# Optimization experiments

Hardware: AMD Instinct MI355X
Metric: run time of the kernel (lower is better)

Reference implementation:

```python
import jax, jax.numpy as jnp
import numpy as np

EPS = 1e-10


def setup_inputs() -> dict:
    key = jax.random.key(0)
    k1, k2, k3 = jax.random.split(key, 3)
    B, K, M, X, Y = 32, 4, 3, 256, 256
    predictions = jax.random.uniform(k1, (B, K, X, Y), dtype=jnp.float32)
    inputs = jax.random.normal(k2, (B, M, X, Y), dtype=jnp.float32)
    heart = jax.random.randint(k3, (B, 1, X, Y), 0, 2, dtype=jnp.int32)
    return {"predictions": predictions, "inputs": inputs, "heart": heart}


def reference(predictions, inputs, heart):
    # predictions: [B,K,X,Y] soft class maps; inputs: [B,M,X,Y]; heart: [B,1,X,Y] 0/1 ROI
    mask = (heart[:, 0] == 1).astype(predictions.dtype)            # [B,X,Y]
    n = jnp.sum(mask, axis=(-2, -1))                                # [B] masked pixel count
    pred = predictions * mask[:, None]                              # [B,K,X,Y] zero outside ROI
    # alpha[b,k] = mean of pred over masked pixels
    alpha = jnp.sum(pred, axis=(-2, -1)) / n[:, None]               # [B,K]
    s = jnp.sum(pred, axis=(-2, -1)) + EPS                          # [B,K]
    # weighted means mu[b,k,m] = sum(pred*inp)/ (sum(pred)+eps)
    mu = jnp.einsum('bkxy,bmxy->bkm', pred, inputs) / s[:, :, None]  # [B,K,M]
    diff = inputs[:, None] - mu[:, :, :, None, None]                 # [B,K,M,X,Y]
    var = jnp.einsum('bkmxy,bkxy->bkm', diff * diff, pred) / s[:, :, None] + EPS  # [B,K,M]
    # Gaussian pdf per (k,m), product over channels m (done in log-space, same math)
    v = var[:, :, :, None, None]
    log_pdf = -0.5 * jnp.log(2.0 * jnp.pi * v) - (diff * diff) / (2.0 * v)  # [B,K,M,X,Y]
    g = jnp.exp(jnp.sum(log_pdf, axis=2))                            # [B,K,X,Y] = prod_m pdf
    mix = jnp.sum(alpha[:, :, None, None] * g, axis=1)               # [B,X,Y]
    ll = jnp.log(mix + EPS)                                          # [B,X,Y]
    # mean of -log-likelihood over masked pixels per batch, then mean over batch
    per_b = -jnp.sum(mask * ll, axis=(-2, -1)) / n                   # [B]
    return jnp.mean(per_b)
```

## Files before the change

kernel.cpp:

```cpp
#include <hip/hip_runtime.h>

#define EPSF 1e-10f

constexpr int B = 32, K = 4, M = 3;
constexpr int NPIX = 256 * 256;
constexpr int BLOCKS_PER_B = 8;
constexpr int THREADS = 256;
constexpr int WAVES = THREADS / 64;
constexpr int CHUNKS = NPIX / (BLOCKS_PER_B * THREADS * 4);
constexpr int NVALS = 1 + K + 2 * K * M;

constexpr int OFF_N     = 0;
constexpr int OFF_W     = OFF_N + B;
constexpr int OFF_P     = OFF_W + B * K;
constexpr int OFF_Q     = OFF_P + B * K * M;
constexpr int OFF_ALPHA = OFF_Q + B * K * M;
constexpr int OFF_MU    = OFF_ALPHA + B * K;
constexpr int OFF_IV    = OFF_MU + B * K * M;
constexpr int OFF_CST   = OFF_IV + B * K * M;
constexpr int OFF_LL    = OFF_CST + B * K;
constexpr int WS_FLOATS = OFF_LL + B;

__device__ __forceinline__ float wave_reduce(float v) {
    #pragma unroll
    for (int off = 32; off > 0; off >>= 1) v += __shfl_down(v, off, 64);
    return v;
}

__global__ __launch_bounds__(THREADS) void pass1_kernel(
    const float* __restrict__ pred, const float* __restrict__ xin,
    const int* __restrict__ heart, float* __restrict__ ws) {
    const int b  = blockIdx.x / BLOCKS_PER_B;
    const int cb = blockIdx.x % BLOCKS_PER_B;

    float nacc = 0.0f;
    float Wk[K] = {};
    float Pa[K][M] = {};
    float Qa[K][M] = {};

    for (int it = 0; it < CHUNKS; ++it) {
        const int p0 = (((cb * CHUNKS + it) * THREADS) + threadIdx.x) * 4;

        const int4 h4 = *(const int4*)(heart + b * NPIX + p0);
        float mk[4];
        mk[0] = (h4.x == 1) ? 1.0f : 0.0f;
        mk[1] = (h4.y == 1) ? 1.0f : 0.0f;
        mk[2] = (h4.z == 1) ? 1.0f : 0.0f;
        mk[3] = (h4.w == 1) ? 1.0f : 0.0f;
        nacc += (mk[0] + mk[1]) + (mk[2] + mk[3]);

        float xv[M][4];
        #pragma unroll
        for (int m = 0; m < M; ++m) {
            float4 t = *(const float4*)(xin + (b * M + m) * NPIX + p0);
            xv[m][0] = t.x; xv[m][1] = t.y; xv[m][2] = t.z; xv[m][3] = t.w;
        }

        #pragma unroll
        for (int k = 0; k < K; ++k) {
            float4 pr = *(const float4*)(pred + (b * K + k) * NPIX + p0);
            float pm[4];
            pm[0] = pr.x * mk[0]; pm[1] = pr.y * mk[1];
            pm[2] = pr.z * mk[2]; pm[3] = pr.w * mk[3];
            Wk[k] += (pm[0] + pm[1]) + (pm[2] + pm[3]);
            #pragma unroll
            for (int m = 0; m < M; ++m) {
                #pragma unroll
                for (int j = 0; j < 4; ++j) {
                    float px = pm[j] * xv[m][j];
                    Pa[k][m] += px;
                    Qa[k][m] += px * xv[m][j];
                }
            }
        }
    }

    float vals[NVALS];
    vals[0] = nacc;
    #pragma unroll
    for (int k = 0; k < K; ++k) vals[1 + k] = Wk[k];
    #pragma unroll
    for (int k = 0; k < K; ++k)
        #pragma unroll
        for (int m = 0; m < M; ++m) {
            vals[1 + K + k * M + m]         = Pa[k][m];
            vals[1 + K + K * M + k * M + m] = Qa[k][m];
        }

    __shared__ float red[WAVES * NVALS];
    #pragma unroll
    for (int i = 0; i < NVALS; ++i) vals[i] = wave_reduce(vals[i]);
    const int wave = threadIdx.x >> 6;
    if ((threadIdx.x & 63) == 0) {
        #pragma unroll
        for (int i = 0; i < NVALS; ++i) red[wave * NVALS + i] = vals[i];
    }
    __syncthreads();
    const int i = threadIdx.x;
    if (i < NVALS) {
        float s = red[i];
        #pragma unroll
        for (int w = 1; w < WAVES; ++w) s += red[w * NVALS + i];
        int dst;
        if (i == 0)            dst = OFF_N + b;
        else if (i < 1 + K)    dst = OFF_W + b * K + (i - 1);
        else if (i < 1 + K + K * M) dst = OFF_P + b * K * M + (i - 1 - K);
        else                   dst = OFF_Q + b * K * M + (i - 1 - K - K * M);
        atomicAdd(&ws[dst], s);
    }
}

__global__ __launch_bounds__(128) void params_kernel(float* __restrict__ ws) {
    const int t = threadIdx.x;
    if (t >= B * K) return;
    const int b = t / K;
    const float n = ws[OFF_N + b];
    const float W = ws[OFF_W + t];
    const float s = W + EPSF;
    ws[OFF_ALPHA + t] = W / n;
    float cst = 0.0f;
    #pragma unroll
    for (int m = 0; m < M; ++m) {
        const float Pv = ws[OFF_P + t * M + m];
        const float Qv = ws[OFF_Q + t * M + m];
        const float mu = Pv / s;
        const float var = (Qv - 2.0f * mu * Pv + mu * mu * W) / s + EPSF;
        ws[OFF_MU + t * M + m] = mu;
        ws[OFF_IV + t * M + m] = 0.5f / var;
        cst -= 0.5f * logf(6.2831853071795864f * var);
    }
    ws[OFF_CST + t] = cst;
}

__global__ __launch_bounds__(THREADS) void pass2_kernel(
    const float* __restrict__ xin, const int* __restrict__ heart,
    float* __restrict__ ws) {
    const int b  = blockIdx.x / BLOCKS_PER_B;
    const int cb = blockIdx.x % BLOCKS_PER_B;

    float alpha[K], cst[K], mu[K][M], iv[K][M];
    #pragma unroll
    for (int k = 0; k < K; ++k) {
        alpha[k] = ws[OFF_ALPHA + b * K + k];
        cst[k]   = ws[OFF_CST + b * K + k];
        #pragma unroll
        for (int m = 0; m < M; ++m) {
            mu[k][m] = ws[OFF_MU + (b * K + k) * M + m];
            iv[k][m] = ws[OFF_IV + (b * K + k) * M + m];
        }
    }

    float acc = 0.0f;
    for (int it = 0; it < CHUNKS; ++it) {
        const int p0 = (((cb * CHUNKS + it) * THREADS) + threadIdx.x) * 4;

        const int4 h4 = *(const int4*)(heart + b * NPIX + p0);
        int hv[4] = {h4.x, h4.y, h4.z, h4.w};

        float xv[M][4];
        #pragma unroll
        for (int m = 0; m < M; ++m) {
            float4 t = *(const float4*)(xin + (b * M + m) * NPIX + p0);
            xv[m][0] = t.x; xv[m][1] = t.y; xv[m][2] = t.z; xv[m][3] = t.w;
        }

        #pragma unroll
        for (int j = 0; j < 4; ++j) {
            float mix = EPSF;
            #pragma unroll
            for (int k = 0; k < K; ++k) {
                float lp = cst[k];
                #pragma unroll
                for (int m = 0; m < M; ++m) {
                    float d = xv[m][j] - mu[k][m];
                    lp -= d * d * iv[k][m];
                }
                mix += alpha[k] * __expf(lp);
            }
            float mask = (hv[j] == 1) ? 1.0f : 0.0f;
            acc += mask * __logf(mix);
        }
    }

    __shared__ float red[WAVES];
    acc = wave_reduce(acc);
    const int wave = threadIdx.x >> 6;
    if ((threadIdx.x & 63) == 0) red[wave] = acc;
    __syncthreads();
    if (threadIdx.x == 0) {
        float s = red[0];
        #pragma unroll
        for (int w = 1; w < WAVES; ++w) s += red[w];
        atomicAdd(&ws[OFF_LL + b], s);
    }
}

__global__ void final_kernel(const float* __restrict__ ws, float* __restrict__ out) {
    if (threadIdx.x == 0 && blockIdx.x == 0) {
        float r = 0.0f;
        for (int b = 0; b < B; ++b) r += -ws[OFF_LL + b] / ws[OFF_N + b];
        out[0] = r / (float)B;
    }
}

extern "C" void kernel_launch(void* const* d_in, const int* in_sizes, int n_in,
                              void* d_out, int out_size, void* d_ws, size_t ws_size,
                              hipStream_t stream) {
    const float* pred  = (const float*)d_in[0];
    const float* xin   = (const float*)d_in[1];
    const int*   heart = (const int*)d_in[2];
    float* out = (float*)d_out;
    float* ws  = (float*)d_ws;

    hipMemsetAsync(d_ws, 0, WS_FLOATS * sizeof(float), stream);
    pass1_kernel<<<B * BLOCKS_PER_B, THREADS, 0, stream>>>(pred, xin, heart, ws);
    params_kernel<<<1, 128, 0, stream>>>(ws);
    pass2_kernel<<<B * BLOCKS_PER_B, THREADS, 0, stream>>>(xin, heart, ws);
    final_kernel<<<1, 64, 0, stream>>>(ws, out);
}
```

Measured before the change: 111.6 us.

## Quadruple grid, replace atomics with per-block partials, fold params into pass2

Raises blocks per batch from 8 to 32 to fill the GPU. Pass1 now writes per-block partial sums instead of atomics, which removes the workspace memset. The separate params kernel is dropped, and each pass2 block reduces the partials and computes the mixture parameters itself. The final kernel reduces in parallel across lanes. The cost is redundant parameter computation in every pass2 block.

```diff
diff --git a/kernel.cpp b/kernel.cpp
--- a/kernel.cpp
+++ b/kernel.cpp
@@ -4,22 +4,16 @@
 
 constexpr int B = 32, K = 4, M = 3;
 constexpr int NPIX = 256 * 256;
-constexpr int BLOCKS_PER_B = 8;
+constexpr int BLOCKS_PER_B = 32;
+constexpr int GRID = B * BLOCKS_PER_B;
 constexpr int THREADS = 256;
 constexpr int WAVES = THREADS / 64;
 constexpr int CHUNKS = NPIX / (BLOCKS_PER_B * THREADS * 4);
 constexpr int NVALS = 1 + K + 2 * K * M;
 
-constexpr int OFF_N     = 0;
-constexpr int OFF_W     = OFF_N + B;
-constexpr int OFF_P     = OFF_W + B * K;
-constexpr int OFF_Q     = OFF_P + B * K * M;
-constexpr int OFF_ALPHA = OFF_Q + B * K * M;
-constexpr int OFF_MU    = OFF_ALPHA + B * K;
-constexpr int OFF_IV    = OFF_MU + B * K * M;
-constexpr int OFF_CST   = OFF_IV + B * K * M;
-constexpr int OFF_LL    = OFF_CST + B * K;
-constexpr int WS_FLOATS = OFF_LL + B;
+constexpr int PSTRIDE  = 32;
+constexpr int OFF_PART = 0;
+constexpr int OFF_LLP  = OFF_PART + GRID * PSTRIDE;
 
 __device__ __forceinline__ float wave_reduce(float v) {
     #pragma unroll
@@ -38,6 +32,7 @@
     float Pa[K][M] = {};
     float Qa[K][M] = {};
 
+    #pragma unroll
     for (int it = 0; it < CHUNKS; ++it) {
         const int p0 = (((cb * CHUNKS + it) * THREADS) + threadIdx.x) * 4;
 
@@ -101,35 +96,8 @@
         float s = red[i];
         #pragma unroll
         for (int w = 1; w < WAVES; ++w) s += red[w * NVALS + i];
-        int dst;
-        if (i == 0)            dst = OFF_N + b;
-        else if (i < 1 + K)    dst = OFF_W + b * K + (i - 1);
-        else if (i < 1 + K + K * M) dst = OFF_P + b * K * M + (i - 1 - K);
-        else                   dst = OFF_Q + b * K * M + (i - 1 - K - K * M);
-        atomicAdd(&ws[dst], s);
-    }
-}
-
-__global__ __launch_bounds__(128) void params_kernel(float* __restrict__ ws) {
-    const int t = threadIdx.x;
-    if (t >= B * K) return;
-    const int b = t / K;
-    const float n = ws[OFF_N + b];
-    const float W = ws[OFF_W + t];
-    const float s = W + EPSF;
-    ws[OFF_ALPHA + t] = W / n;
-    float cst = 0.0f;
-    #pragma unroll
-    for (int m = 0; m < M; ++m) {
-        const float Pv = ws[OFF_P + t * M + m];
-        const float Qv = ws[OFF_Q + t * M + m];
-        const float mu = Pv / s;
-        const float var = (Qv - 2.0f * mu * Pv + mu * mu * W) / s + EPSF;
-        ws[OFF_MU + t * M + m] = mu;
-        ws[OFF_IV + t * M + m] = 0.5f / var;
-        cst -= 0.5f * logf(6.2831853071795864f * var);
-    }
-    ws[OFF_CST + t] = cst;
+        ws[OFF_PART + blockIdx.x * PSTRIDE + i] = s;
+    }
 }
 
 __global__ __launch_bounds__(THREADS) void pass2_kernel(
@@ -138,19 +106,41 @@
     const int b  = blockIdx.x / BLOCKS_PER_B;
     const int cb = blockIdx.x % BLOCKS_PER_B;
 
-    float alpha[K], cst[K], mu[K][M], iv[K][M];
-    #pragma unroll
-    for (int k = 0; k < K; ++k) {
-        alpha[k] = ws[OFF_ALPHA + b * K + k];
-        cst[k]   = ws[OFF_CST + b * K + k];
-        #pragma unroll
-        for (int m = 0; m < M; ++m) {
-            mu[k][m] = ws[OFF_MU + (b * K + k) * M + m];
-            iv[k][m] = ws[OFF_IV + (b * K + k) * M + m];
+    __shared__ float raw[NVALS];
+    if (threadIdx.x < NVALS) {
+        const float* base = ws + OFF_PART + (b * BLOCKS_PER_B) * PSTRIDE + threadIdx.x;
+        float s = 0.0f;
+        #pragma unroll
+        for (int c = 0; c < BLOCKS_PER_B; ++c) s += base[c * PSTRIDE];
+        raw[threadIdx.x] = s;
+    }
+    __syncthreads();
+
+    float alpha[K], cstk[K], mu[K][M], iv[K][M];
+    {
+        const float n = raw[0];
+        #pragma unroll
+        for (int k = 0; k < K; ++k) {
+            const float W = raw[1 + k];
+            const float s = W + EPSF;
+            alpha[k] = W / n;
+            float cst = 0.0f;
+            #pragma unroll
+            for (int m = 0; m < M; ++m) {
+                const float Pv = raw[1 + K + k * M + m];
+                const float Qv = raw[1 + K + K * M + k * M + m];
+                const float muv = Pv / s;
+                const float var = (Qv - 2.0f * muv * Pv + muv * muv * W) / s + EPSF;
+                mu[k][m] = muv;
+                iv[k][m] = 0.5f / var;
+                cst -= 0.5f * logf(6.2831853071795864f * var);
+            }
+            cstk[k] = cst;
         }
     }
 
     float acc = 0.0f;
+    #pragma unroll
     for (int it = 0; it < CHUNKS; ++it) {
         const int p0 = (((cb * CHUNKS + it) * THREADS) + threadIdx.x) * 4;
 
@@ -169,7 +159,7 @@
             float mix = EPSF;
             #pragma unroll
             for (int k = 0; k < K; ++k) {
-                float lp = cst[k];
+                float lp = cstk[k];
                 #pragma unroll
                 for (int m = 0; m < M; ++m) {
                     float d = xv[m][j] - mu[k][m];
@@ -182,25 +172,32 @@
         }
     }
 
-    __shared__ float red[WAVES];
+    __shared__ float red2[WAVES];
     acc = wave_reduce(acc);
-    const int wave = threadIdx.x >> 6;
-    if ((threadIdx.x & 63) == 0) red[wave] = acc;
+    if ((threadIdx.x & 63) == 0) red2[threadIdx.x >> 6] = acc;
     __syncthreads();
     if (threadIdx.x == 0) {
-        float s = red[0];
-        #pragma unroll
-        for (int w = 1; w < WAVES; ++w) s += red[w];
-        atomicAdd(&ws[OFF_LL + b], s);
+        float s = red2[0];
+        #pragma unroll
+        for (int w = 1; w < WAVES; ++w) s += red2[w];
+        ws[OFF_LLP + blockIdx.x] = s;
     }
 }
 
 __global__ void final_kernel(const float* __restrict__ ws, float* __restrict__ out) {
-    if (threadIdx.x == 0 && blockIdx.x == 0) {
-        float r = 0.0f;
-        for (int b = 0; b < B; ++b) r += -ws[OFF_LL + b] / ws[OFF_N + b];
-        out[0] = r / (float)B;
-    }
+    const int lane = threadIdx.x;
+    float r = 0.0f;
+    if (lane < B) {
+        float ll = 0.0f, n = 0.0f;
+        #pragma unroll
+        for (int c = 0; c < BLOCKS_PER_B; ++c) {
+            ll += ws[OFF_LLP + lane * BLOCKS_PER_B + c];
+            n  += ws[OFF_PART + (lane * BLOCKS_PER_B + c) * PSTRIDE + 0];
+        }
+        r = -ll / n;
+    }
+    r = wave_reduce(r);
+    if (lane == 0) out[0] = r / (float)B;
 }
 
 extern "C" void kernel_launch(void* const* d_in, const int* in_sizes, int n_in,
@@ -212,9 +209,7 @@
     float* out = (float*)d_out;
     float* ws  = (float*)d_ws;
 
-    hipMemsetAsync(d_ws, 0, WS_FLOATS * sizeof(float), stream);
-    pass1_kernel<<<B * BLOCKS_PER_B, THREADS, 0, stream>>>(pred, xin, heart, ws);
-    params_kernel<<<1, 128, 0, stream>>>(ws);
-    pass2_kernel<<<B * BLOCKS_PER_B, THREADS, 0, stream>>>(xin, heart, ws);
+    pass1_kernel<<<GRID, THREADS, 0, stream>>>(pred, xin, heart, ws);
+    pass2_kernel<<<GRID, THREADS, 0, stream>>>(xin, heart, ws);
     final_kernel<<<1, 64, 0, stream>>>(ws, out);
 }
```

New measurement: 111.9 us (median of 2 runs). About the same (+0.3%).
